# Optimization experiments

Hardware: AMD Instinct MI355X
Metric: run time of the kernel (lower is better)

Reference implementation:

```python
import jax, jax.numpy as jnp
import numpy as np

GRID = 100  # voxel index range per axis (coors drawn in [0, GRID))
N_POINTS = 1_000_000
N_FEAT = 64
MAX_VOXELS = N_POINTS  # static upper bound on number of unique voxels


def setup_inputs() -> dict:
    key = jax.random.key(0)
    kf, kc = jax.random.split(key)
    feats = jax.random.normal(kf, (N_POINTS, N_FEAT), dtype=jnp.float32)
    coors = jax.random.randint(kc, (N_POINTS, 3), 0, GRID, dtype=jnp.int32)
    return {"feats": feats, "coors": coors}


def reference(feats, coors):
    """Dynamic point-to-voxel scatter with 'mean' reduce (average_points=True).

    Returns (voxel_feats [M_max, C], voxel_coors [M_max, 3]).
    Unique-voxel rows are packed first (sorted by linear key); padded rows
    (beyond the true voxel count M) have zero features and coors == -1.
    """
    n = feats.shape[0]
    # linear hash of 3D voxel coordinate
    keys = (coors[:, 0].astype(jnp.int64) * GRID * GRID
            + coors[:, 1].astype(jnp.int64) * GRID
            + coors[:, 2].astype(jnp.int64))
    uniq, inv = jnp.unique(keys, size=MAX_VOXELS, fill_value=-1,
                           return_inverse=True)
    inv = inv.reshape(n)
    # per-voxel sum and count -> mean
    sums = jax.ops.segment_sum(feats, inv, num_segments=MAX_VOXELS)
    counts = jax.ops.segment_sum(jnp.ones((n,), dtype=feats.dtype), inv,
                                 num_segments=MAX_VOXELS)
    voxel_feats = sums / jnp.maximum(counts, 1.0)[:, None]
    # decode unique linear keys back to 3D voxel coordinates (-1 for padding)
    valid = uniq >= 0
    u = jnp.where(valid, uniq, 0)
    cx = (u // (GRID * GRID)).astype(jnp.int32)
    cy = ((u // GRID) % GRID).astype(jnp.int32)
    cz = (u % GRID).astype(jnp.int32)
    voxel_coors = jnp.stack([cx, cy, cz], axis=-1)
    voxel_coors = jnp.where(valid[:, None], voxel_coors, -1)
    voxel_feats = jnp.where(valid[:, None], voxel_feats, 0.0)
    return voxel_feats, voxel_coors
```

## Files before the change

kernel.cpp:

```cpp
#include <hip/hip_runtime.h>

#define NPTS   1000000
#define NFEAT  64
#define GRIDN  100
#define NBINS  1000000

#define SCAN_B    256
#define SCAN_I    4
#define SCAN_TILE 1024
#define NBLK      977

typedef float f4 __attribute__((ext_vector_type(4)));

__global__ __launch_bounds__(256) void k_count(const int4* __restrict__ coors4,
                                               int4* __restrict__ keys4,
                                               int* __restrict__ count, int nq) {
    int t = blockIdx.x * blockDim.x + threadIdx.x;
    if (t >= nq) return;
    int4 a = coors4[3 * t + 0];
    int4 b = coors4[3 * t + 1];
    int4 c = coors4[3 * t + 2];
    int k0 = (a.x * GRIDN + a.y) * GRIDN + a.z;
    int k1 = (a.w * GRIDN + b.x) * GRIDN + b.y;
    int k2 = (b.z * GRIDN + b.w) * GRIDN + c.x;
    int k3 = (c.y * GRIDN + c.z) * GRIDN + c.w;
    keys4[t] = make_int4(k0, k1, k2, k3);
    atomicAdd(&count[k0], 1);
    atomicAdd(&count[k1], 1);
    atomicAdd(&count[k2], 1);
    atomicAdd(&count[k3], 1);
}

__global__ __launch_bounds__(256) void k_scan1(const int4* __restrict__ count4,
                                               int* __restrict__ blkOcc,
                                               int* __restrict__ blkCnt) {
    __shared__ int sO[SCAN_B], sC[SCAN_B];
    int tid  = threadIdx.x;
    int base = blockIdx.x * SCAN_TILE + tid * SCAN_I;
    int tO = 0, tC = 0;
    if (base < NBINS) {
        int4 v = count4[base >> 2];
        tO = (v.x > 0) + (v.y > 0) + (v.z > 0) + (v.w > 0);
        tC = v.x + v.y + v.z + v.w;
    }
    sO[tid] = tO; sC[tid] = tC;
    __syncthreads();
    for (int ofs = SCAN_B / 2; ofs > 0; ofs >>= 1) {
        if (tid < ofs) { sO[tid] += sO[tid + ofs]; sC[tid] += sC[tid + ofs]; }
        __syncthreads();
    }
    if (tid == 0) { blkOcc[blockIdx.x] = sO[0]; blkCnt[blockIdx.x] = sC[0]; }
}

__global__ __launch_bounds__(1024) void k_scan2(int* __restrict__ blkOcc,
                                                int* __restrict__ blkCnt,
                                                int* __restrict__ m_dev) {
    __shared__ int sO[1024], sC[1024];
    int tid = threadIdx.x;
    int vO = (tid < NBLK) ? blkOcc[tid] : 0;
    int vC = (tid < NBLK) ? blkCnt[tid] : 0;
    sO[tid] = vO; sC[tid] = vC;
    __syncthreads();
    for (int ofs = 1; ofs < 1024; ofs <<= 1) {
        int a = 0, b = 0;
        if (tid >= ofs) { a = sO[tid - ofs]; b = sC[tid - ofs]; }
        __syncthreads();
        sO[tid] += a; sC[tid] += b;
        __syncthreads();
    }
    if (tid < NBLK) {
        blkOcc[tid] = sO[tid] - vO;
        blkCnt[tid] = sC[tid] - vC;
    }
    if (tid == 1023) *m_dev = sO[1023];
}

__global__ __launch_bounds__(256) void k_scan3(const int4* __restrict__ count4,
                                               int4* __restrict__ pstart4,
                                               const int* __restrict__ blkOcc,
                                               const int* __restrict__ blkCnt,
                                               long long* __restrict__ rankstart,
                                               int4* __restrict__ rowinfo) {
    __shared__ int sO[SCAN_B], sC[SCAN_B];
    int tid  = threadIdx.x;
    int base = blockIdx.x * SCAN_TILE + tid * SCAN_I;
    int4 v = make_int4(0, 0, 0, 0);
    if (base < NBINS) v = count4[base >> 2];
    int c[SCAN_I] = {v.x, v.y, v.z, v.w};
    int locO[SCAN_I], locC[SCAN_I];
    int tO = 0, tC = 0;
    #pragma unroll
    for (int i = 0; i < SCAN_I; ++i) {
        locO[i] = tO; locC[i] = tC;
        tO += (c[i] > 0) ? 1 : 0;
        tC += c[i];
    }
    sO[tid] = tO; sC[tid] = tC;
    __syncthreads();
    for (int ofs = 1; ofs < SCAN_B; ofs <<= 1) {
        int a = 0, b = 0;
        if (tid >= ofs) { a = sO[tid - ofs]; b = sC[tid - ofs]; }
        __syncthreads();
        sO[tid] += a; sC[tid] += b;
        __syncthreads();
    }
    if (base >= NBINS) return;
    int exO = sO[tid] - tO + blkOcc[blockIdx.x];
    int exC = sC[tid] - tC + blkCnt[blockIdx.x];
    int4 ps;
    ps.x = exC + locC[0]; ps.y = exC + locC[1];
    ps.z = exC + locC[2]; ps.w = exC + locC[3];
    pstart4[base >> 2] = ps;
    int psa[SCAN_I] = {ps.x, ps.y, ps.z, ps.w};
    #pragma unroll
    for (int i = 0; i < SCAN_I; ++i) {
        if (c[i] > 0) {
            int bin = base + i;
            int r   = exO + locO[i];
            rankstart[bin] = ((long long)r << 32)
                           | (long long)(unsigned)((c[i] << 20) | psa[i]);
            *(int2*)(&rowinfo[r]) = make_int2(psa[i], bin | (c[i] << 20));
        }
    }
}

__global__ __launch_bounds__(256) void k_fill(const int4* __restrict__ keys4,
                                              int* __restrict__ pstart,
                                              const long long* __restrict__ rankstart,
                                              int* __restrict__ perm,
                                              int4* __restrict__ rowinfo, int nq) {
    int t = blockIdx.x * blockDim.x + threadIdx.x;
    if (t >= nq) return;
    int4 kv = keys4[t];
    int ks[4] = {kv.x, kv.y, kv.z, kv.w};
    long long rs[4];
    #pragma unroll
    for (int i = 0; i < 4; ++i) rs[i] = rankstart[ks[i]];
    int pbase = t * 4;
    #pragma unroll
    for (int i = 0; i < 4; ++i) {
        int start = (int)(rs[i] & 0xFFFFF);
        int cnt   = (int)((rs[i] >> 20) & 0xFFF);
        int r     = (int)(rs[i] >> 32);
        int p     = pbase + i;
        if (cnt == 1) {
            ((int*)rowinfo)[r * 4 + 2] = p;
        } else {
            int pos = atomicAdd(&pstart[ks[i]], 1);
            int j = pos - start;
            if (j < 2) ((int*)rowinfo)[r * 4 + 2 + j] = p;
            else       perm[pos] = p;
        }
    }
}

__global__ __launch_bounds__(256) void k_mean(const f4* __restrict__ feats4,
                                              const int4* __restrict__ rowinfo,
                                              const int* __restrict__ perm,
                                              const int* __restrict__ m_dev,
                                              f4* __restrict__ out4) {
    int gid = blockIdx.x * blockDim.x + threadIdx.x;
    int row = gid >> 4;
    int sub = gid & 15;
    if (row >= NBINS) return;
    float* out_coors = (float*)(out4 + (size_t)NBINS * 16);
    int M = *m_dev;
    if (row < M) {
        int4 info = rowinfo[row];
        int start = info.x;
        int bin   = info.y & 0xFFFFF;
        int cnt   = info.y >> 20;
        f4 s = __builtin_nontemporal_load(&feats4[(size_t)info.z * 16 + sub]);
        if (cnt > 1) {
            f4 f = __builtin_nontemporal_load(&feats4[(size_t)info.w * 16 + sub]);
            s += f;
        }
        if (cnt > 2) {
            int gbase = (threadIdx.x & 63) & ~15;
            for (int b0 = 2; b0 < cnt; b0 += 16) {
                int rem = cnt - b0;
                int lim = rem < 16 ? rem : 16;
                int pv  = (sub < lim) ? perm[start + b0 + sub] : 0;
                for (int j = 0; j < lim; ++j) {
                    int pj = __shfl(pv, gbase + j);
                    f4 f = __builtin_nontemporal_load(&feats4[(size_t)pj * 16 + sub]);
                    s += f;
                }
            }
        }
        float inv = 1.0f / (float)cnt;
        s *= inv;
        __builtin_nontemporal_store(s, &out4[(size_t)row * 16 + sub]);
        if (sub < 3) {
            int v = (sub == 0) ? bin / (GRIDN * GRIDN)
                  : (sub == 1) ? (bin / GRIDN) % GRIDN
                  :               bin % GRIDN;
            out_coors[row * 3 + sub] = (float)v;
        }
    } else {
        f4 z = (f4){0.f, 0.f, 0.f, 0.f};
        __builtin_nontemporal_store(z, &out4[(size_t)row * 16 + sub]);
        if (sub < 3) out_coors[row * 3 + sub] = -1.f;
    }
}

extern "C" void kernel_launch(void* const* d_in, const int* in_sizes, int n_in,
                              void* d_out, int out_size, void* d_ws, size_t ws_size,
                              hipStream_t stream) {
    const float* feats = (const float*)d_in[0];
    const int*   coors = (const int*)d_in[1];
    float*       out   = (float*)d_out;
    int n = in_sizes[1] / 3;

    int*       keys      = (int*)d_ws;
    int*       count     = keys   + NPTS;
    int*       pstart    = count  + NBINS;
    int*       perm      = pstart + NBINS;
    int4*      rowinfo   = (int4*)(perm + NPTS);
    long long* rankstart = (long long*)(rowinfo + NBINS);
    int*       blkOcc    = (int*)(rankstart + NBINS);
    int*       blkCnt    = blkOcc + NBLK;
    int*       m_dev     = blkCnt + NBLK;

    hipMemsetAsync(count, 0, NBINS * sizeof(int), stream);

    int b  = 256;
    int nq = n >> 2;
    k_count<<<(nq + b - 1) / b, b, 0, stream>>>((const int4*)coors, (int4*)keys,
                                                count, nq);
    k_scan1<<<NBLK, SCAN_B, 0, stream>>>((const int4*)count, blkOcc, blkCnt);
    k_scan2<<<1, 1024, 0, stream>>>(blkOcc, blkCnt, m_dev);
    k_scan3<<<NBLK, SCAN_B, 0, stream>>>((const int4*)count, (int4*)pstart,
                                         blkOcc, blkCnt, rankstart, rowinfo);
    k_fill<<<(nq + b - 1) / b, b, 0, stream>>>((const int4*)keys, pstart, rankstart,
                                               perm, rowinfo, nq);
    k_mean<<<(NBINS * 16) / b, b, 0, stream>>>((const f4*)feats, rowinfo, perm,
                                               m_dev, (f4*)out);
}
```

Baseline: 537.6 us.

## Replace three-pass scan with single-pass decoupled look-back scan

Merges the reduce, block-prefix and downsweep scan kernels into one kernel that uses decoupled look-back. Each block publishes its aggregate and inclusive prefix through packed 64-bit status words, and a wavefront polls its predecessors. This removes two kernel launches and one re-read of the count array. It also adds nontemporal loads and stores in the counting kernel. The look-back depends on blocks being scheduled in order and adds spin-waiting, and the 21-bit fields cap the prefix values.

```diff
diff --git a/kernel.cpp b/kernel.cpp
--- a/kernel.cpp
+++ b/kernel.cpp
@@ -9,83 +9,48 @@
 #define SCAN_I    4
 #define SCAN_TILE 1024
 #define NBLK      977
+#define NBLK_PAD  1024
 
 typedef float f4 __attribute__((ext_vector_type(4)));
-
-__global__ __launch_bounds__(256) void k_count(const int4* __restrict__ coors4,
-                                               int4* __restrict__ keys4,
+typedef int   i4 __attribute__((ext_vector_type(4)));
+
+#define PACK_ST(st, o, cc) ( ((unsigned long long)(st) << 62) \
+                           | ((unsigned long long)(unsigned)(o) << 21) \
+                           | (unsigned long long)(unsigned)(cc) )
+
+__global__ __launch_bounds__(256) void k_count(const i4* __restrict__ coors4,
+                                               i4* __restrict__ keys4,
                                                int* __restrict__ count, int nq) {
     int t = blockIdx.x * blockDim.x + threadIdx.x;
     if (t >= nq) return;
-    int4 a = coors4[3 * t + 0];
-    int4 b = coors4[3 * t + 1];
-    int4 c = coors4[3 * t + 2];
+    i4 a = __builtin_nontemporal_load(&coors4[3 * t + 0]);
+    i4 b = __builtin_nontemporal_load(&coors4[3 * t + 1]);
+    i4 c = __builtin_nontemporal_load(&coors4[3 * t + 2]);
     int k0 = (a.x * GRIDN + a.y) * GRIDN + a.z;
     int k1 = (a.w * GRIDN + b.x) * GRIDN + b.y;
     int k2 = (b.z * GRIDN + b.w) * GRIDN + c.x;
     int k3 = (c.y * GRIDN + c.z) * GRIDN + c.w;
-    keys4[t] = make_int4(k0, k1, k2, k3);
+    i4 kv = {k0, k1, k2, k3};
+    __builtin_nontemporal_store(kv, &keys4[t]);
     atomicAdd(&count[k0], 1);
     atomicAdd(&count[k1], 1);
     atomicAdd(&count[k2], 1);
     atomicAdd(&count[k3], 1);
 }
 
-__global__ __launch_bounds__(256) void k_scan1(const int4* __restrict__ count4,
-                                               int* __restrict__ blkOcc,
-                                               int* __restrict__ blkCnt) {
+__global__ __launch_bounds__(256) void k_scan(const i4* __restrict__ count4,
+                                              i4* __restrict__ pstart4,
+                                              unsigned long long* __restrict__ tstate,
+                                              long long* __restrict__ rankstart,
+                                              int4* __restrict__ rowinfo,
+                                              int* __restrict__ m_dev) {
     __shared__ int sO[SCAN_B], sC[SCAN_B];
+    __shared__ int sBaseO, sBaseC;
     int tid  = threadIdx.x;
-    int base = blockIdx.x * SCAN_TILE + tid * SCAN_I;
-    int tO = 0, tC = 0;
-    if (base < NBINS) {
-        int4 v = count4[base >> 2];
-        tO = (v.x > 0) + (v.y > 0) + (v.z > 0) + (v.w > 0);
-        tC = v.x + v.y + v.z + v.w;
-    }
-    sO[tid] = tO; sC[tid] = tC;
-    __syncthreads();
-    for (int ofs = SCAN_B / 2; ofs > 0; ofs >>= 1) {
-        if (tid < ofs) { sO[tid] += sO[tid + ofs]; sC[tid] += sC[tid + ofs]; }
-        __syncthreads();
-    }
-    if (tid == 0) { blkOcc[blockIdx.x] = sO[0]; blkCnt[blockIdx.x] = sC[0]; }
-}
-
-__global__ __launch_bounds__(1024) void k_scan2(int* __restrict__ blkOcc,
-                                                int* __restrict__ blkCnt,
-                                                int* __restrict__ m_dev) {
-    __shared__ int sO[1024], sC[1024];
-    int tid = threadIdx.x;
-    int vO = (tid < NBLK) ? blkOcc[tid] : 0;
-    int vC = (tid < NBLK) ? blkCnt[tid] : 0;
-    sO[tid] = vO; sC[tid] = vC;
-    __syncthreads();
-    for (int ofs = 1; ofs < 1024; ofs <<= 1) {
-        int a = 0, b = 0;
-        if (tid >= ofs) { a = sO[tid - ofs]; b = sC[tid - ofs]; }
-        __syncthreads();
-        sO[tid] += a; sC[tid] += b;
-        __syncthreads();
-    }
-    if (tid < NBLK) {
-        blkOcc[tid] = sO[tid] - vO;
-        blkCnt[tid] = sC[tid] - vC;
-    }
-    if (tid == 1023) *m_dev = sO[1023];
-}
-
-__global__ __launch_bounds__(256) void k_scan3(const int4* __restrict__ count4,
-                                               int4* __restrict__ pstart4,
-                                               const int* __restrict__ blkOcc,
-                                               const int* __restrict__ blkCnt,
-                                               long long* __restrict__ rankstart,
-                                               int4* __restrict__ rowinfo) {
-    __shared__ int sO[SCAN_B], sC[SCAN_B];
-    int tid  = threadIdx.x;
-    int base = blockIdx.x * SCAN_TILE + tid * SCAN_I;
-    int4 v = make_int4(0, 0, 0, 0);
-    if (base < NBINS) v = count4[base >> 2];
+    int blk  = blockIdx.x;
+    int base = blk * SCAN_TILE + tid * SCAN_I;
+    i4 v = {0, 0, 0, 0};
+    if (base < NBINS) v = __builtin_nontemporal_load(&count4[base >> 2]);
     int c[SCAN_I] = {v.x, v.y, v.z, v.w};
     int locO[SCAN_I], locC[SCAN_I];
     int tO = 0, tC = 0;
@@ -104,12 +69,70 @@
         sO[tid] += a; sC[tid] += b;
         __syncthreads();
     }
+    int aggO = sO[SCAN_B - 1], aggC = sC[SCAN_B - 1];
+    if (blk == 0) {
+        if (tid == 0) {
+            __hip_atomic_store(&tstate[0], PACK_ST(2, aggO, aggC),
+                               __ATOMIC_RELAXED, __HIP_MEMORY_SCOPE_AGENT);
+            sBaseO = 0; sBaseC = 0;
+        }
+    } else {
+        if (tid == 0)
+            __hip_atomic_store(&tstate[blk], PACK_ST(1, aggO, aggC),
+                               __ATOMIC_RELAXED, __HIP_MEMORY_SCOPE_AGENT);
+        if (tid < 64) {
+            int lane = tid;
+            int exO = 0, exC = 0;
+            int wend = blk - 1;
+            for (;;) {
+                int j = wend - lane;
+                unsigned long long s = (j >= 0)
+                    ? __hip_atomic_load(&tstate[j], __ATOMIC_RELAXED,
+                                        __HIP_MEMORY_SCOPE_AGENT)
+                    : PACK_ST(2, 0, 0);
+                unsigned st = (unsigned)(s >> 62);
+                unsigned long long b2 = __ballot(st == 2u);
+                unsigned long long b0 = __ballot(st == 0u);
+                if (b2) {
+                    int L = __ffsll((unsigned long long)b2) - 1;
+                    unsigned long long need =
+                        (L >= 63) ? ~0ull : ((1ull << (L + 1)) - 1ull);
+                    if (b0 & need) { __builtin_amdgcn_s_sleep(1); continue; }
+                    int o  = (lane <= L) ? (int)((s >> 21) & 0x1FFFFF) : 0;
+                    int cc = (lane <= L) ? (int)(s & 0x1FFFFF) : 0;
+                    #pragma unroll
+                    for (int ofs = 32; ofs > 0; ofs >>= 1) {
+                        o  += __shfl_down(o, ofs);
+                        cc += __shfl_down(cc, ofs);
+                    }
+                    exO += o; exC += cc;
+                    break;
+                } else {
+                    if (b0) { __builtin_amdgcn_s_sleep(1); continue; }
+                    int o  = (int)((s >> 21) & 0x1FFFFF);
+                    int cc = (int)(s & 0x1FFFFF);
+                    #pragma unroll
+                    for (int ofs = 32; ofs > 0; ofs >>= 1) {
+                        o  += __shfl_down(o, ofs);
+                        cc += __shfl_down(cc, ofs);
+                    }
+                    exO += o; exC += cc;
+                    wend -= 64;
+                }
+            }
+            if (lane == 0) {
+                __hip_atomic_store(&tstate[blk], PACK_ST(2, exO + aggO, exC + aggC),
+                                   __ATOMIC_RELAXED, __HIP_MEMORY_SCOPE_AGENT);
+                sBaseO = exO; sBaseC = exC;
+                if (blk == NBLK - 1) *m_dev = exO + aggO;
+            }
+        }
+    }
+    __syncthreads();
     if (base >= NBINS) return;
-    int exO = sO[tid] - tO + blkOcc[blockIdx.x];
-    int exC = sC[tid] - tC + blkCnt[blockIdx.x];
-    int4 ps;
-    ps.x = exC + locC[0]; ps.y = exC + locC[1];
-    ps.z = exC + locC[2]; ps.w = exC + locC[3];
+    int exO = sBaseO + sO[tid] - tO;
+    int exC = sBaseC + sC[tid] - tC;
+    i4 ps = {exC + locC[0], exC + locC[1], exC + locC[2], exC + locC[3]};
     pstart4[base >> 2] = ps;
     int psa[SCAN_I] = {ps.x, ps.y, ps.z, ps.w};
     #pragma unroll
@@ -124,14 +147,14 @@
     }
 }
 
-__global__ __launch_bounds__(256) void k_fill(const int4* __restrict__ keys4,
+__global__ __launch_bounds__(256) void k_fill(const i4* __restrict__ keys4,
                                               int* __restrict__ pstart,
                                               const long long* __restrict__ rankstart,
                                               int* __restrict__ perm,
                                               int4* __restrict__ rowinfo, int nq) {
     int t = blockIdx.x * blockDim.x + threadIdx.x;
     if (t >= nq) return;
-    int4 kv = keys4[t];
+    i4 kv = keys4[t];
     int ks[4] = {kv.x, kv.y, kv.z, kv.w};
     long long rs[4];
     #pragma unroll
@@ -212,27 +235,26 @@
     float*       out   = (float*)d_out;
     int n = in_sizes[1] / 3;
 
-    int*       keys      = (int*)d_ws;
-    int*       count     = keys   + NPTS;
-    int*       pstart    = count  + NBINS;
-    int*       perm      = pstart + NBINS;
-    int4*      rowinfo   = (int4*)(perm + NPTS);
-    long long* rankstart = (long long*)(rowinfo + NBINS);
-    int*       blkOcc    = (int*)(rankstart + NBINS);
-    int*       blkCnt    = blkOcc + NBLK;
-    int*       m_dev     = blkCnt + NBLK;
-
-    hipMemsetAsync(count, 0, NBINS * sizeof(int), stream);
+    int*                keys      = (int*)d_ws;
+    int*                count     = keys   + NPTS;
+    unsigned long long* tstate    = (unsigned long long*)(count + NBINS);
+    int*                pstart    = (int*)(tstate + NBLK_PAD);
+    int*                perm      = pstart + NBINS;
+    int4*               rowinfo   = (int4*)(perm + NPTS);
+    long long*          rankstart = (long long*)(rowinfo + NBINS);
+    int*                m_dev     = (int*)(rankstart + NBINS);
+
+    (void)hipMemsetAsync(count, 0,
+                   NBINS * sizeof(int) + NBLK_PAD * sizeof(unsigned long long),
+                   stream);
 
     int b  = 256;
     int nq = n >> 2;
-    k_count<<<(nq + b - 1) / b, b, 0, stream>>>((const int4*)coors, (int4*)keys,
+    k_count<<<(nq + b - 1) / b, b, 0, stream>>>((const i4*)coors, (i4*)keys,
                                                 count, nq);
-    k_scan1<<<NBLK, SCAN_B, 0, stream>>>((const int4*)count, blkOcc, blkCnt);
-    k_scan2<<<1, 1024, 0, stream>>>(blkOcc, blkCnt, m_dev);
-    k_scan3<<<NBLK, SCAN_B, 0, stream>>>((const int4*)count, (int4*)pstart,
-                                         blkOcc, blkCnt, rankstart, rowinfo);
-    k_fill<<<(nq + b - 1) / b, b, 0, stream>>>((const int4*)keys, pstart, rankstart,
+    k_scan<<<NBLK, SCAN_B, 0, stream>>>((const i4*)count, (i4*)pstart, tstate,
+                                        rankstart, rowinfo, m_dev);
+    k_fill<<<(nq + b - 1) / b, b, 0, stream>>>((const i4*)keys, pstart, rankstart,
                                                perm, rowinfo, nq);
     k_mean<<<(NBINS * 16) / b, b, 0, stream>>>((const f4*)feats, rowinfo, perm,
                                                m_dev, (f4*)out);
```

New measurement: 532.9 us. About the same (-0.9%).
